# Optimization experiments

Measured on AMD Instinct MI355X. Metric: run time of the kernel, lower is better.

## Reference

```python
import jax, jax.numpy as jnp
import numpy as np

M_PARAM = 8          # M from __init__
NUM_INTERESTS = 32   # K, num_extracted_interests (max)


def setup_inputs() -> dict:
    key = jax.random.key(0)
    ks = jax.random.split(key, 6)
    bs, L, N, d, ic, K = 512, 100, 64, 256, 256, NUM_INTERESTS
    history = jax.random.normal(ks[0], (bs, L, d), dtype=jnp.float32)
    history_mask = jnp.ones((bs, L), dtype=bool)  # unused by the original forward, kept for signature fidelity
    candidates = jax.random.normal(ks[1], (bs, N, d), dtype=jnp.float32)
    num_extracted_interests = jnp.maximum(
        jax.random.randint(ks[2], (bs,), 0, K, dtype=jnp.int32), 1)
    unique_category_counts = jax.random.randint(ks[3], (bs,), 1, 19, dtype=jnp.int32)
    W = jax.random.normal(ks[4], (ic, d), dtype=jnp.float32) / np.sqrt(d)   # Linear(news_dim->interest_dim), no bias
    context_codes = jax.random.normal(ks[5], (K, ic), dtype=jnp.float32) / np.sqrt(ic)
    return {
        "history_news_representations": history,
        "history_mask": history_mask,
        "candidate_news_representations": candidates,
        "num_extracted_interests": num_extracted_interests,
        "unique_category_counts": unique_category_counts,
        "W": W,
        "context_codes": context_codes,
    }


def _user_encoder(history, candidates, num_interests, cat_counts, W, context_codes):
    bs, L, d = history.shape
    K = context_codes.shape[0]
    # ---- PolyAttention ----
    proj = jnp.tanh(jnp.einsum('bld,cd->blc', history, W))           # [bs, L, ic]
    scores = jnp.einsum('blc,kc->bkl', proj, context_codes)          # [bs, K, L]
    code_mask = jnp.arange(K)[None, :] < num_interests[:, None]      # [bs, K]
    scores = jnp.where(code_mask[:, :, None], scores, jnp.float32(-1e9))
    attn = jax.nn.softmax(scores, axis=2)                            # over history length L
    attn = jnp.nan_to_num(attn, nan=0.0, posinf=0.0, neginf=0.0)
    interests = jnp.einsum('bkl,bld->bkd', attn, history)            # [bs, K, d]
    # ---- InterestCandidateAttention, vectorized over all N candidates ----
    w = jnp.einsum('bkd,bnd->bnk', interests, candidates)            # [bs, N, K]
    dynK = jnp.clip(
        jnp.ceil(jnp.log2(M_PARAM * cat_counts.astype(jnp.float32))).astype(jnp.int32),
        1, K)                                                        # [bs]
    # variable-K top-k mask via descending ranks (values a.s. distinct)
    order = jnp.argsort(-w, axis=-1)
    ranks = jnp.argsort(order, axis=-1)                              # rank 0 = largest
    topk_mask = (ranks < dynK[:, None, None]).astype(w.dtype)        # [bs, N, K]
    masked = w * topk_mask
    user = jnp.einsum('bnk,bkd->bnd', masked, interests)             # [bs, N, d]
    return user


def reference(history_news_representations, history_mask, candidate_news_representations,
              num_extracted_interests, unique_category_counts, W, context_codes):
    return _user_encoder(history_news_representations, candidate_news_representations,
                         num_extracted_interests, unique_category_counts, W, context_codes)
```

## Files before the change

kernel.cpp:

```cpp
#include <hip/hip_runtime.h>
#include <hip/hip_bf16.h>

typedef __bf16 bf16_t;
typedef __bf16 bf16x8 __attribute__((ext_vector_type(8)));
typedef float  f32x4  __attribute__((ext_vector_type(4)));

#define BS 512
#define LH 100
#define NC 64
#define DD 256
#define IC 256
#define KK 32

#define OFF_WPL 6553600
#define OFF_CPL (6553600 + 3 * 131072)

__device__ __forceinline__ void split3(float v, bf16_t& h, bf16_t& l, bf16_t& l2) {
    h = (bf16_t)v;  float r1 = v - (float)h;
    l = (bf16_t)r1; float r2 = r1 - (float)l;
    l2 = (bf16_t)r2;
}

__device__ __forceinline__ void split3x8(const float* v, bf16x8& h, bf16x8& l, bf16x8& l2) {
#pragma unroll
    for (int j = 0; j < 8; j++) {
        bf16_t a, b, c;
        split3(v[j], a, b, c);
        h[j] = a; l[j] = b; l2[j] = c;
    }
}

__device__ __forceinline__ void mfma6(const bf16x8& ah, const bf16x8& al, const bf16x8& al2,
                                      const bf16x8& bh, const bf16x8& bl, const bf16x8& bl2,
                                      f32x4& accM, f32x4& accC) {
    accM = __builtin_amdgcn_mfma_f32_16x16x32_bf16(ah,  bh,  accM, 0, 0, 0);
    accC = __builtin_amdgcn_mfma_f32_16x16x32_bf16(ah,  bl,  accC, 0, 0, 0);
    accC = __builtin_amdgcn_mfma_f32_16x16x32_bf16(al,  bh,  accC, 0, 0, 0);
    accC = __builtin_amdgcn_mfma_f32_16x16x32_bf16(ah,  bl2, accC, 0, 0, 0);
    accC = __builtin_amdgcn_mfma_f32_16x16x32_bf16(al,  bl,  accC, 0, 0, 0);
    accC = __builtin_amdgcn_mfma_f32_16x16x32_bf16(al2, bh,  accC, 0, 0, 0);
}

__device__ __forceinline__ float fast_tanh_f32(float xf) {
    const double t  = fabs((double)xf) * 2.0;
    const double nf = rint(t * 1.4426950408889634);
    double r = fma(nf, -6.93147180369123816490e-01, t);
    r = fma(nf, -1.90821492927058770002e-10, r);
    const double r2 = r * r;
    double p =        2.08767569878680989792e-09;
    p = fma(p, r,     2.50521083854417187751e-08);
    p = fma(p, r,     2.75573192239858906526e-07);
    p = fma(p, r,     2.75573192239858925110e-06);
    p = fma(p, r,     2.48015873015873015873e-05);
    p = fma(p, r,     1.98412698412698412526e-04);
    p = fma(p, r,     1.38888888888888894069e-03);
    p = fma(p, r,     8.33333333333333321769e-03);
    p = fma(p, r,     4.16666666666666643537e-02);
    p = fma(p, r,     1.66666666666666657415e-01);
    p = fma(p, r,     5.00000000000000000000e-01);
    const double q   = fma(r2, p, r);
    const double s   = ldexp(1.0, (int)nf);
    const double em1 = fma(s, q, s - 1.0);
    double ti = em1 / (em1 + 2.0);
    if (t > 20.0) ti = 1.0;
    return copysignf((float)ti, xf);
}

__global__ __launch_bounds__(256) void kp_split(const float* __restrict__ W,
                                                const float* __restrict__ C,
                                                bf16_t* __restrict__ Wh, bf16_t* __restrict__ Wl,
                                                bf16_t* __restrict__ Wl2,
                                                bf16_t* __restrict__ Ch, bf16_t* __restrict__ Cl,
                                                bf16_t* __restrict__ Cl2) {
    int idx = blockIdx.x * 256 + threadIdx.x;
    if (idx < 65536) {
        bf16_t h, l, l2;
        split3(W[idx], h, l, l2);
        Wh[idx] = h; Wl[idx] = l; Wl2[idx] = l2;
    } else {
        int i = idx - 65536;
        if (i < 8192) {
            bf16_t h, l, l2;
            split3(C[i], h, l, l2);
            Ch[i] = h; Cl[i] = l; Cl2[i] = l2;
        }
    }
}

#define WROW 280
__global__ __launch_bounds__(448) void k12_proj_scores(const float* __restrict__ H,
                                                       const bf16_t* __restrict__ Wh,
                                                       const bf16_t* __restrict__ Wl,
                                                       const bf16_t* __restrict__ Wl2,
                                                       const bf16_t* __restrict__ Ch,
                                                       const bf16_t* __restrict__ Cl,
                                                       const bf16_t* __restrict__ Cl2,
                                                       float* __restrict__ S) {
    __shared__ bf16_t wlds[3 * 16 * WROW];
    __shared__ float  pl[7][16 * 34];

    const int tid = threadIdx.x;
    const int wave = tid >> 6;
    const int lane = tid & 63;
    const int r = lane & 15, q = lane >> 4;
    const int b = blockIdx.x;
    const int lrow0 = wave * 16;

    bf16x8 Ah[8], Al[8], Al2[8];
    {
        long grow = (long)b * LH + lrow0 + r;
        const long maxrow = (long)BS * LH - 1;
        if (grow > maxrow) grow = maxrow;
        const float* arow = H + (size_t)grow * DD + q * 8;
#pragma unroll
        for (int ks = 0; ks < 8; ks++) {
            const float* ap = arow + ks * 32;
            float4 u = *(const float4*)ap;
            float4 v = *(const float4*)(ap + 4);
            float av[8] = {u.x, u.y, u.z, u.w, v.x, v.y, v.z, v.w};
            split3x8(av, Ah[ks], Al[ks], Al2[ks]);
        }
    }

    const f32x4 zero = {0.f, 0.f, 0.f, 0.f};
    f32x4 saccM[2], saccC[2];
    saccM[0] = zero; saccM[1] = zero; saccC[0] = zero; saccC[1] = zero;

    float* myp = pl[wave];

    for (int c16 = 0; c16 < 16; c16++) {
        const int w0 = c16 * 16;
        __syncthreads();
        for (int g = tid; g < 1536; g += 448) {
            const int p = g >> 9, rem = g & 511, row = rem >> 5, grp = rem & 31;
            const bf16_t* src = (p == 0) ? Wh : (p == 1) ? Wl : Wl2;
            bf16x8 v = *(const bf16x8*)(src + (size_t)(w0 + row) * DD + grp * 8);
            *(bf16x8*)(wlds + (p * 16 + row) * WROW + grp * 8) = v;
        }
        __syncthreads();

        f32x4 aM = zero, aC = zero;
#pragma unroll
        for (int ks = 0; ks < 8; ks++) {
            const int rowb = r * WROW + ks * 32 + q * 8;
            bf16x8 bh  = *(const bf16x8*)(wlds + 0 * 16 * WROW + rowb);
            bf16x8 bl  = *(const bf16x8*)(wlds + 1 * 16 * WROW + rowb);
            bf16x8 bl2 = *(const bf16x8*)(wlds + 2 * 16 * WROW + rowb);
            mfma6(Ah[ks], Al[ks], Al2[ks], bh, bl, bl2, aM, aC);
        }

        const int colb = (c16 & 1) * 16;
#pragma unroll
        for (int i = 0; i < 4; i++) {
            float s1 = aM[i] + aC[i];
            myp[(q * 4 + i) * 34 + colb + r] = fast_tanh_f32(s1);
        }

        if (c16 & 1) {
            const int c0 = (c16 >> 1) * 32;
            const float* ps = myp + r * 34 + q * 8;
            float pv[8];
#pragma unroll
            for (int j = 0; j < 8; j++) pv[j] = ps[j];
            bf16x8 ph, plo, pl2;
            split3x8(pv, ph, plo, pl2);
#pragma unroll
            for (int ntS = 0; ntS < 2; ntS++) {
                const size_t base = (size_t)(ntS * 16 + r) * IC + c0 + q * 8;
                bf16x8 ch  = *(const bf16x8*)(Ch  + base);
                bf16x8 cl  = *(const bf16x8*)(Cl  + base);
                bf16x8 cl2 = *(const bf16x8*)(Cl2 + base);
                mfma6(ph, plo, pl2, ch, cl, cl2, saccM[ntS], saccC[ntS]);
            }
        }
    }

#pragma unroll
    for (int ntS = 0; ntS < 2; ntS++)
#pragma unroll
        for (int i = 0; i < 4; i++) {
            const int lrow = lrow0 + q * 4 + i;
            if (lrow < LH)
                S[((size_t)b * LH + lrow) * KK + ntS * 16 + r] = saccM[ntS][i] + saccC[ntS][i];
        }
}

__global__ __launch_bounds__(512) void k3456_fused(const float* __restrict__ Sg,
                                                   const int* __restrict__ ni,
                                                   const int* __restrict__ cc,
                                                   const float* __restrict__ H,
                                                   const float* __restrict__ cand,
                                                   float* __restrict__ out) {
    __shared__ __align__(16) char smem[47616];
    float*  attn_l = (float*)smem;
    float*  ls     = (float*)(smem + 12800);
    double* red    = (double*)(smem + 25600);
    float*  ht     = (float*)(smem + 12800);
    float*  I_l    = (float*)(smem + 12800);
    float*  shw    = (float*)smem;

    const int b = blockIdx.x;
    const int tid = threadIdx.x;
    const int wave = tid >> 6;
    const int lane = tid & 63;
    const int r = lane & 15, q = lane >> 4;
    const f32x4 zero = {0.f, 0.f, 0.f, 0.f};

    {
        const float* Sb = Sg + (size_t)b * LH * KK;
        for (int i = tid; i < LH * KK; i += 512) ls[i] = Sb[i];
        __syncthreads();

        const int k = tid & 31;
        const int grp = tid >> 5;
        const bool act = (grp < 8);
        const int nib = ni[b];

        double vals[13];
        int cnt = 0;
        if (act) {
            double vmax = -1e300;
            for (int l = grp; l < LH; l += 8) {
                double v = (double)ls[l * KK + k];
                vals[cnt++] = v;
                vmax = fmax(vmax, v);
            }
            red[grp * 33 + k] = vmax;
        }
        __syncthreads();
        if (tid < 32) {
            double m = red[k];
            for (int j = 1; j < 8; j++) m = fmax(m, red[j * 33 + k]);
            red[k] = m;
        }
        __syncthreads();
        const double mx = red[k];
        __syncthreads();

        if (act) {
            double s = 0.0;
            for (int i = 0; i < cnt; i++) {
                double e = exp(vals[i] - mx);
                vals[i] = e;
                s += e;
            }
            red[grp * 33 + k] = s;
        }
        __syncthreads();
        if (tid < 32) {
            double t = 0.0;
            for (int j = 0; j < 8; j++) t += red[j * 33 + k];
            red[k] = t;
        }
        __syncthreads();
        const double inv = 1.0 / red[k];

        if (act) {
            float* ab = attn_l + k * LH;
            const bool masked = (k >= nib);
            cnt = 0;
            for (int l = grp; l < LH; l += 8) {
                ab[l] = masked ? 0.01f : (float)(vals[cnt] * inv);
                cnt++;
            }
        }
    }
    __syncthreads();

    {
        const float* Hb = H + (size_t)b * LH * DD;
        const int mtB = wave & 1;
        const int m0B = mtB * 16;

        f32x4 accM[4], accC[4];
#pragma unroll
        for (int jj = 0; jj < 4; jj++) { accM[jj] = zero; accC[jj] = zero; }

        for (int ks = 0; ks < 4; ks++) {
            const int l0c = ks * 32;
            __syncthreads();
            for (int u = tid; u < 32 * 64; u += 512) {
                const int l = u >> 6, dg = u & 63;
                float4 v = {0.f, 0.f, 0.f, 0.f};
                if (l0c + l < LH) v = *(const float4*)(Hb + (size_t)(l0c + l) * DD + dg * 4);
                ht[(dg * 4 + 0) * 34 + l] = v.x;
                ht[(dg * 4 + 1) * 34 + l] = v.y;
                ht[(dg * 4 + 2) * 34 + l] = v.z;
                ht[(dg * 4 + 3) * 34 + l] = v.w;
            }
            __syncthreads();

            float av[8];
#pragma unroll
            for (int j = 0; j < 8; j++) {
                const int l = l0c + q * 8 + j;
                av[j] = (l < LH) ? attn_l[(m0B + r) * LH + l] : 0.f;
            }
            bf16x8 ah, al, al2;
            split3x8(av, ah, al, al2);

#pragma unroll
            for (int jj = 0; jj < 4; jj++) {
                const int job = wave + jj * 8;
                const int nt = job >> 1;
                const int n0 = nt * 16;
                float bv[8];
                const float* hp = ht + (n0 + r) * 34 + q * 8;
#pragma unroll
                for (int j = 0; j < 8; j++) bv[j] = hp[j];
                bf16x8 bh, bl, bl2;
                split3x8(bv, bh, bl, bl2);
                mfma6(ah, al, al2, bh, bl, bl2, accM[jj], accC[jj]);
            }
        }
        __syncthreads();

#pragma unroll
        for (int jj = 0; jj < 4; jj++) {
            const int job = wave + jj * 8;
            const int nt = job >> 1;
            const int n0 = nt * 16;
#pragma unroll
            for (int i = 0; i < 4; i++)
                I_l[(m0B + q * 4 + i) * 260 + n0 + r] = accM[jj][i] + accC[jj][i];
        }
    }
    __syncthreads();

    {
        const float* Cb = cand + (size_t)b * NC * DD;
        const int job = wave;
        const int mt = job >> 1, nt = job & 1;
        const int m0 = mt * 16, n0 = nt * 16;
        f32x4 accM = zero, accC = zero;
#pragma unroll
        for (int ks = 0; ks < 8; ks++) {
            const float* ap = Cb + (size_t)(m0 + r) * DD + ks * 32 + q * 8;
            const float* bp = I_l + (n0 + r) * 260 + ks * 32 + q * 8;
            float4 u1 = *(const float4*)ap;      float4 u2 = *(const float4*)(ap + 4);
            float4 v1 = *(const float4*)bp;      float4 v2 = *(const float4*)(bp + 4);
            float av[8] = {u1.x,u1.y,u1.z,u1.w,u2.x,u2.y,u2.z,u2.w};
            float bv[8] = {v1.x,v1.y,v1.z,v1.w,v2.x,v2.y,v2.z,v2.w};
            bf16x8 ah, al, al2, bh, bl, bl2;
            split3x8(av, ah, al, al2);
            split3x8(bv, bh, bl, bl2);
            mfma6(ah, al, al2, bh, bl, bl2, accM, accC);
        }
#pragma unroll
        for (int i = 0; i < 4; i++) shw[(m0 + q * 4 + i) * 33 + n0 + r] = accM[i] + accC[i];

        __syncthreads();

        if (tid < NC) {
            const int n = tid;
            int c8 = 8 * cc[b];
            int dynK = 32 - __clz(c8 - 1);
            dynK = min(max(dynK, 1), KK);
            float v[KK];
            for (int k = 0; k < KK; k++) v[k] = shw[n * 33 + k];
            for (int k = 0; k < KK; k++) {
                int rank = 0;
                for (int j = 0; j < KK; j++)
                    rank += (v[j] > v[k]) || (v[j] == v[k] && j < k);
                shw[n * 33 + k] = (rank < dynK) ? v[k] : 0.f;
            }
        }
    }
    __syncthreads();

    {
        const int d = tid & 255;
        const int nh = tid >> 8;
        float icol[KK];
#pragma unroll
        for (int k = 0; k < KK; k++) icol[k] = I_l[k * 260 + d];

        const int nend = nh * 32 + 32;
        for (int n = nh * 32; n < nend; n++) {
            const float* wr = shw + n * 33;
            float acc = 0.f;
#pragma unroll
            for (int k = 0; k < KK; k++) acc += wr[k] * icol[k];
            out[((size_t)b * NC + n) * DD + d] = acc;
        }
    }
}

extern "C" void kernel_launch(void* const* d_in, const int* in_sizes, int n_in,
                              void* d_out, int out_size, void* d_ws, size_t ws_size,
                              hipStream_t stream) {
    const float* hist = (const float*)d_in[0];
    const float* cand = (const float*)d_in[2];
    const int* ni = (const int*)d_in[3];
    const int* cc = (const int*)d_in[4];
    const float* W = (const float*)d_in[5];
    const float* C = (const float*)d_in[6];
    float* out = (float*)d_out;

    char* w8 = (char*)d_ws;
    float*  S   = (float*)(w8 + 0);
    bf16_t* Wh  = (bf16_t*)(w8 + OFF_WPL);
    bf16_t* Wl  = (bf16_t*)(w8 + OFF_WPL + 131072);
    bf16_t* Wl2 = (bf16_t*)(w8 + OFF_WPL + 262144);
    bf16_t* Ch  = (bf16_t*)(w8 + OFF_CPL);
    bf16_t* Cl  = (bf16_t*)(w8 + OFF_CPL + 16384);
    bf16_t* Cl2 = (bf16_t*)(w8 + OFF_CPL + 32768);

    kp_split<<<288, 256, 0, stream>>>(W, C, Wh, Wl, Wl2, Ch, Cl, Cl2);
    k12_proj_scores<<<BS, 448, 0, stream>>>(hist, Wh, Wl, Wl2, Ch, Cl, Cl2, S);
    k3456_fused<<<BS, 512, 0, stream>>>(S, ni, cc, hist, cand, out);
}
```

Before: 286.5 us.

## Double-buffer W tiles in LDS with register prefetch and XOR swizzle

```diff
diff --git a/kernel.cpp b/kernel.cpp
--- a/kernel.cpp
+++ b/kernel.cpp
@@ -87,7 +87,7 @@
     }
 }
 
-#define WROW 280
+#define WCH 24576
 __global__ __launch_bounds__(448) void k12_proj_scores(const float* __restrict__ H,
                                                        const bf16_t* __restrict__ Wh,
                                                        const bf16_t* __restrict__ Wl,
@@ -96,8 +96,8 @@
                                                        const bf16_t* __restrict__ Cl,
                                                        const bf16_t* __restrict__ Cl2,
                                                        float* __restrict__ S) {
-    __shared__ bf16_t wlds[3 * 16 * WROW];
-    __shared__ float  pl[7][16 * 34];
+    __shared__ __align__(16) char wbuf[2][WCH];
+    __shared__ float pl[7][16 * 34];
 
     const int tid = threadIdx.x;
     const int wave = tid >> 6;
@@ -106,6 +106,18 @@
     const int b = blockIdx.x;
     const int lrow0 = wave * 16;
 
+    const bf16_t* it_base[4];
+    int it_src[4], it_dst[4];
+#pragma unroll
+    for (int it = 0; it < 4; it++) {
+        const int g = tid + it * 448;
+        const int p = (g >> 9) & 3, rem = g & 511, row = rem >> 5, grp = rem & 31;
+        it_base[it] = (p == 0) ? Wh : (p == 1) ? Wl : Wl2;
+        it_src[it] = row * DD + grp * 8;
+        it_dst[it] = (p * 16 + row) * 512 + ((grp * 16) ^ ((row & 7) << 4));
+    }
+    const bool has4 = (tid < 192);
+
     bf16x8 Ah[8], Al[8], Al2[8];
     {
         long grow = (long)b * LH + lrow0 + r;
@@ -127,33 +139,51 @@
     saccM[0] = zero; saccM[1] = zero; saccC[0] = zero; saccC[1] = zero;
 
     float* myp = pl[wave];
+    const int swz = (r & 7) << 4;
+
+    {
+        bf16x8 p0 = *(const bf16x8*)(it_base[0] + it_src[0]);
+        bf16x8 p1 = *(const bf16x8*)(it_base[1] + it_src[1]);
+        bf16x8 p2 = *(const bf16x8*)(it_base[2] + it_src[2]);
+        bf16x8 p3;
+        if (has4) p3 = *(const bf16x8*)(it_base[3] + it_src[3]);
+        *(bf16x8*)(wbuf[0] + it_dst[0]) = p0;
+        *(bf16x8*)(wbuf[0] + it_dst[1]) = p1;
+        *(bf16x8*)(wbuf[0] + it_dst[2]) = p2;
+        if (has4) *(bf16x8*)(wbuf[0] + it_dst[3]) = p3;
+    }
+    __syncthreads();
 
     for (int c16 = 0; c16 < 16; c16++) {
-        const int w0 = c16 * 16;
-        __syncthreads();
-        for (int g = tid; g < 1536; g += 448) {
-            const int p = g >> 9, rem = g & 511, row = rem >> 5, grp = rem & 31;
-            const bf16_t* src = (p == 0) ? Wh : (p == 1) ? Wl : Wl2;
-            bf16x8 v = *(const bf16x8*)(src + (size_t)(w0 + row) * DD + grp * 8);
-            *(bf16x8*)(wlds + (p * 16 + row) * WROW + grp * 8) = v;
-        }
-        __syncthreads();
+        const char* cur = wbuf[c16 & 1];
+        char* nxt = wbuf[(c16 & 1) ^ 1];
+        const bool pfv = (c16 < 15);
+
+        bf16x8 p0, p1, p2, p3;
+        if (pfv) {
+            const int co = (c16 + 1) * 16 * DD;
+            p0 = *(const bf16x8*)(it_base[0] + co + it_src[0]);
+            p1 = *(const bf16x8*)(it_base[1] + co + it_src[1]);
+            p2 = *(const bf16x8*)(it_base[2] + co + it_src[2]);
+            if (has4) p3 = *(const bf16x8*)(it_base[3] + co + it_src[3]);
+        }
 
         f32x4 aM = zero, aC = zero;
 #pragma unroll
         for (int ks = 0; ks < 8; ks++) {
-            const int rowb = r * WROW + ks * 32 + q * 8;
-            bf16x8 bh  = *(const bf16x8*)(wlds + 0 * 16 * WROW + rowb);
-            bf16x8 bl  = *(const bf16x8*)(wlds + 1 * 16 * WROW + rowb);
-            bf16x8 bl2 = *(const bf16x8*)(wlds + 2 * 16 * WROW + rowb);
+            const int colb = (ks * 64 + q * 16) ^ swz;
+            const char* rowp = cur + r * 512 + colb;
+            bf16x8 bh  = *(const bf16x8*)(rowp);
+            bf16x8 bl  = *(const bf16x8*)(rowp + 8192);
+            bf16x8 bl2 = *(const bf16x8*)(rowp + 16384);
             mfma6(Ah[ks], Al[ks], Al2[ks], bh, bl, bl2, aM, aC);
         }
 
-        const int colb = (c16 & 1) * 16;
+        const int colb2 = (c16 & 1) * 16;
 #pragma unroll
         for (int i = 0; i < 4; i++) {
             float s1 = aM[i] + aC[i];
-            myp[(q * 4 + i) * 34 + colb + r] = fast_tanh_f32(s1);
+            myp[(q * 4 + i) * 34 + colb2 + r] = fast_tanh_f32(s1);
         }
 
         if (c16 & 1) {
@@ -173,6 +203,14 @@
                 mfma6(ph, plo, pl2, ch, cl, cl2, saccM[ntS], saccC[ntS]);
             }
         }
+
+        if (pfv) {
+            *(bf16x8*)(nxt + it_dst[0]) = p0;
+            *(bf16x8*)(nxt + it_dst[1]) = p1;
+            *(bf16x8*)(nxt + it_dst[2]) = p2;
+            if (has4) *(bf16x8*)(nxt + it_dst[3]) = p3;
+        }
+        __syncthreads();
     }
 
 #pragma unroll
```

Measured after the change: 251.4 us. 1.14x faster.
